# Kernel tuning notes

Hardware: AMD Instinct MI355X
Metric: run time of the kernel (lower is better)

Reference implementation:

```python
import jax, jax.numpy as jnp
import numpy as np

N = 100000
E = 1_600_000
IN_X, OUT_X = 128, 128
IN_E, OUT_E = 32, 128


def setup_inputs() -> dict:
    key = jax.random.key(0)
    k1, k2, k3, k4, k5, k6, k7 = jax.random.split(key, 7)
    x = jax.random.normal(k1, (N, IN_X), dtype=jnp.float32)
    edge_index = jax.random.randint(k2, (2, E), 0, N, dtype=jnp.int64)
    edge_attr = jax.random.normal(k3, (E, IN_E), dtype=jnp.float32)
    Wx = jax.random.normal(k4, (IN_X, OUT_X), dtype=jnp.float32) * (1.0 / np.sqrt(IN_X))
    bx = jax.random.normal(k5, (OUT_X,), dtype=jnp.float32) * 0.01
    We = jax.random.normal(k6, (IN_E, OUT_E), dtype=jnp.float32) * (1.0 / np.sqrt(IN_E))
    be = jax.random.normal(k7, (OUT_E,), dtype=jnp.float32) * 0.01
    return {"x": x, "edge_index": edge_index, "edge_attr": edge_attr,
            "Wx": Wx, "bx": bx, "We": We, "be": be}


def reference(x, edge_index, edge_attr, Wx, bx, We, be):
    # torch: to_dense() -> [N, N, in_e]; sum over dim=1 == scatter-add of
    # edge_attr into rows indexed by the source node edge_index[0].
    agg = jax.ops.segment_sum(edge_attr, edge_index[0], num_segments=x.shape[0])  # [N, in_e]
    hx = x @ Wx + bx          # [N, out_x]
    he = agg @ We + be        # [N, out_e]
    return jnp.concatenate((hx, he), axis=1)  # [N, out_x + out_e]
```

## Files before the change

kernel.cpp:

```cpp
#include <hip/hip_runtime.h>


#define BSHIFT    7
#define BSIZE     128
#define NBMAX     1024
#define SEG_CAP   3584
#define POOL_SZ   3648
#define CHUNK_A   8192
#define SPILL_CAP 65536

typedef short bf16x8 __attribute__((ext_vector_type(8)));
typedef float f32x4  __attribute__((ext_vector_type(4)));

__device__ __forceinline__ unsigned short f2bf(float f) {
    union { float f; unsigned u; } c; c.f = f;
    unsigned u = c.u;
    u += 0x7FFF + ((u >> 16) & 1);
    return (unsigned short)(u >> 16);
}

__global__ __launch_bounds__(512) void binA_kernel(
    const int* __restrict__ src, int E, int nb,
    unsigned* __restrict__ segs, int* __restrict__ gcnt,
    int2* __restrict__ spill, int* __restrict__ spillcnt)
{
    __shared__ unsigned pool[CHUNK_A];
    __shared__ int hist[NBMAX];
    __shared__ int offs[NBMAX];
    __shared__ int lcur[NBMAX];
    __shared__ int gbase[NBMAX];
    __shared__ int gallow[NBMAX];
    __shared__ int wsum[8];

    int tid = threadIdx.x;
    int base = blockIdx.x * CHUNK_A;

    for (int i = tid; i < NBMAX; i += 512) hist[i] = 0;
    __syncthreads();

    int srcv[CHUNK_A / 512];
    #pragma unroll
    for (int u = 0; u < CHUNK_A / 512; ++u) {
        int e = base + tid + u * 512;
        int s = (e < E) ? src[e] : -1;
        srcv[u] = s;
        if (s >= 0) atomicAdd(&hist[s >> BSHIFT], 1);
    }
    __syncthreads();

    {
        int t2 = tid * 2;
        int c0 = hist[t2], c1 = hist[t2 + 1];
        int s = c0 + c1;
        int lane = tid & 63, wid = tid >> 6;
        int ws = s;
        #pragma unroll
        for (int d = 1; d < 64; d <<= 1) {
            int t = __shfl_up(ws, d);
            if (lane >= d) ws += t;
        }
        if (lane == 63) wsum[wid] = ws;
        __syncthreads();
        int woff = 0;
        #pragma unroll
        for (int w = 0; w < 8; ++w) if (w < wid) woff += wsum[w];
        int ex = woff + ws - s;
        offs[t2] = ex;          lcur[t2] = ex;
        offs[t2 + 1] = ex + c0; lcur[t2 + 1] = ex + c0;
    }
    __syncthreads();

    {
        int t2 = tid * 2;
        #pragma unroll
        for (int u = 0; u < 2; ++u) {
            int b = t2 + u;
            if (b < nb) {
                int cnt = hist[b];
                int b0 = cnt ? atomicAdd(&gcnt[b], cnt) : 0;
                gbase[b] = b0;
                int allow = SEG_CAP - b0;
                if (allow < 0) allow = 0;
                if (allow > cnt) allow = cnt;
                gallow[b] = allow;
            }
        }
    }
    __syncthreads();

    #pragma unroll
    for (int u = 0; u < CHUNK_A / 512; ++u) {
        int s = srcv[u];
        if (s >= 0) {
            int e = base + tid + u * 512;
            int b = s >> BSHIFT;
            int p = atomicAdd(&lcur[b], 1);
            pool[p] = ((unsigned)e << BSHIFT) | (unsigned)(s & (BSIZE - 1));
        }
    }
    __syncthreads();

    int wid = tid >> 6, lane = tid & 63;
    for (int b = wid; b < nb; b += 8) {
        int cnt = hist[b];
        int off = offs[b];
        int allow = gallow[b];
        unsigned* dst = segs + (size_t)b * SEG_CAP + gbase[b];
        for (int i = lane; i < allow; i += 64)
            dst[i] = pool[off + i];
        int excess = cnt - allow;
        if (excess > 0) {
            int sb;
            if (lane == 0) sb = atomicAdd(spillcnt, excess);
            sb = __shfl(sb, 0);
            for (int i = lane; i < excess; i += 64) {
                int sp = sb + i;
                if (sp < SPILL_CAP) {
                    unsigned pv = pool[off + allow + i];
                    spill[sp] = make_int2((int)(pv >> BSHIFT),
                                          (b << BSHIFT) | (int)(pv & (BSIZE - 1)));
                }
            }
        }
    }
}

__global__ __launch_bounds__(512, 4) void fused_kernel(
    const unsigned* __restrict__ segs, const int* __restrict__ gcnt,
    const int2* __restrict__ spill, const int* __restrict__ spillcnt,
    const float4* __restrict__ ea4, const float* __restrict__ x,
    const float* __restrict__ Wx, const float* __restrict__ bx,
    const float* __restrict__ We, const float* __restrict__ be,
    float* __restrict__ out, int N)
{
    __shared__ int counts[BSIZE];
    __shared__ int starts[BSIZE + 1];
    __shared__ int cursor[BSIZE];
    __shared__ int pool[POOL_SZ];
    __shared__ char sAgg[BSIZE * 64];
    __shared__ char sWeT[128 * 64];
    __shared__ char sWxT[128 * 256];

    int tid = threadIdx.x;
    int b = blockIdx.x;
    int node0 = b << BSHIFT;
    int lane = tid & 63, w = tid >> 6;
    int col = lane & 15, m = lane >> 4;

    if (tid < BSIZE) counts[tid] = 0;
    for (int i = tid; i < 128 * 128; i += 512) {
        int k = i >> 7, j = i & 127;
        *(unsigned short*)(sWxT + j * 256 + ((k * 2) ^ ((j & 7) << 4))) = f2bf(Wx[i]);
    }
    for (int i = tid; i < 32 * 128; i += 512) {
        int k = i >> 7, j = i & 127;
        *(unsigned short*)(sWeT + j * 64 + ((k * 2) ^ ((j & 3) << 4))) = f2bf(We[i]);
    }
    float bxv[8], bev[8];
    #pragma unroll
    for (int ct = 0; ct < 8; ++ct) {
        bxv[ct] = bx[ct * 16 + col];
        bev[ct] = be[ct * 16 + col];
    }
    __syncthreads();

    int segn = gcnt[b]; if (segn > SEG_CAP) segn = SEG_CAP;
    const unsigned* seg = segs + (size_t)b * SEG_CAP;
    int nsp = *spillcnt; if (nsp > SPILL_CAP) nsp = SPILL_CAP;

    for (int i = tid; i < segn; i += 512)
        atomicAdd(&counts[seg[i] & (BSIZE - 1)], 1);
    if (nsp)
        for (int i = tid; i < nsp; i += 512) {
            int2 p = spill[i];
            if ((p.y >> BSHIFT) == b) atomicAdd(&counts[p.y & (BSIZE - 1)], 1);
        }
    __syncthreads();

    if (tid < 64) {
        int c0 = counts[tid * 2], c1 = counts[tid * 2 + 1];
        int s = c0 + c1;
        int ws = s;
        #pragma unroll
        for (int d = 1; d < 64; d <<= 1) {
            int t = __shfl_up(ws, d);
            if (tid >= d) ws += t;
        }
        int ex = ws - s;
        starts[tid * 2] = ex;          cursor[tid * 2] = ex;
        starts[tid * 2 + 1] = ex + c0; cursor[tid * 2 + 1] = ex + c0;
        if (tid == 63) starts[BSIZE] = ws;
    }
    __syncthreads();

    for (int i = tid; i < segn; i += 512) {
        unsigned pe = seg[i];
        int pos = atomicAdd(&cursor[pe & (BSIZE - 1)], 1);
        if (pos < POOL_SZ) pool[pos] = (int)(pe >> BSHIFT);
    }
    if (nsp)
        for (int i = tid; i < nsp; i += 512) {
            int2 p = spill[i];
            if ((p.y >> BSHIFT) == b) {
                int pos = atomicAdd(&cursor[p.y & (BSIZE - 1)], 1);
                if (pos < POOL_SZ) pool[pos] = p.x;
            }
        }
    __syncthreads();

    {
        int g = tid >> 2, q2 = tid & 3;
        int node = node0 + g;
        float4 aL0 = {0.f,0.f,0.f,0.f}, aL1 = {0.f,0.f,0.f,0.f};
        float4 aH0 = {0.f,0.f,0.f,0.f}, aH1 = {0.f,0.f,0.f,0.f};
        if (node < N) {
            int p0 = starts[g], p1 = starts[g + 1];
            if (p1 > POOL_SZ) p1 = POOL_SZ;
            int p = p0;
            for (; p + 4 <= p1; p += 4) {
                int e0 = pool[p], e1 = pool[p + 1], e2 = pool[p + 2], e3 = pool[p + 3];
                const float4* r0 = ea4 + (size_t)e0 * 8;
                const float4* r1 = ea4 + (size_t)e1 * 8;
                const float4* r2 = ea4 + (size_t)e2 * 8;
                const float4* r3 = ea4 + (size_t)e3 * 8;
                float4 l0 = r0[q2],     l1 = r1[q2],     l2 = r2[q2],     l3 = r3[q2];
                float4 h0 = r0[q2 + 4], h1 = r1[q2 + 4], h2 = r2[q2 + 4], h3 = r3[q2 + 4];
                aL0.x += l0.x; aL0.y += l0.y; aL0.z += l0.z; aL0.w += l0.w;
                aL1.x += l1.x; aL1.y += l1.y; aL1.z += l1.z; aL1.w += l1.w;
                aH0.x += h0.x; aH0.y += h0.y; aH0.z += h0.z; aH0.w += h0.w;
                aH1.x += h1.x; aH1.y += h1.y; aH1.z += h1.z; aH1.w += h1.w;
                aL0.x += l2.x; aL0.y += l2.y; aL0.z += l2.z; aL0.w += l2.w;
                aL1.x += l3.x; aL1.y += l3.y; aL1.z += l3.z; aL1.w += l3.w;
                aH0.x += h2.x; aH0.y += h2.y; aH0.z += h2.z; aH0.w += h2.w;
                aH1.x += h3.x; aH1.y += h3.y; aH1.z += h3.z; aH1.w += h3.w;
            }
            for (; p < p1; ++p) {
                const float4* r = ea4 + (size_t)pool[p] * 8;
                float4 l = r[q2], h = r[q2 + 4];
                aL0.x += l.x; aL0.y += l.y; aL0.z += l.z; aL0.w += l.w;
                aH0.x += h.x; aH0.y += h.y; aH0.z += h.z; aH0.w += h.w;
            }
            aL0.x += aL1.x; aL0.y += aL1.y; aL0.z += aL1.z; aL0.w += aL1.w;
            aH0.x += aH1.x; aH0.y += aH1.y; aH0.z += aH1.z; aH0.w += aH1.w;
        }
        uint2 lo, hi;
        lo.x = (unsigned)f2bf(aL0.x) | ((unsigned)f2bf(aL0.y) << 16);
        lo.y = (unsigned)f2bf(aL0.z) | ((unsigned)f2bf(aL0.w) << 16);
        hi.x = (unsigned)f2bf(aH0.x) | ((unsigned)f2bf(aH0.y) << 16);
        hi.y = (unsigned)f2bf(aH0.z) | ((unsigned)f2bf(aH0.w) << 16);
        int swz = (g & 7) << 4;
        *(uint2*)(sAgg + ((g * 64 + q2 * 8) ^ swz))       = lo;
        *(uint2*)(sAgg + ((g * 64 + (q2 + 4) * 8) ^ swz)) = hi;
    }

    int lrow = (w << 4) + col;
    int grow = node0 + lrow;
    bool rok = grow < N;
    int srow = node0 + (w << 4) + m * 4;

    {
        const float* xr = x + (size_t)grow * 128 + m * 8;
        bf16x8 ax[4];
        #pragma unroll
        for (int kk = 0; kk < 4; ++kk) {
            float4 p0 = {0.f,0.f,0.f,0.f}, p1 = {0.f,0.f,0.f,0.f};
            if (rok) {
                p0 = *(const float4*)(xr + kk * 32);
                p1 = *(const float4*)(xr + kk * 32 + 4);
            }
            bf16x8 a;
            a[0] = (short)f2bf(p0.x); a[1] = (short)f2bf(p0.y);
            a[2] = (short)f2bf(p0.z); a[3] = (short)f2bf(p0.w);
            a[4] = (short)f2bf(p1.x); a[5] = (short)f2bf(p1.y);
            a[6] = (short)f2bf(p1.z); a[7] = (short)f2bf(p1.w);
            ax[kk] = a;
        }

        #pragma unroll
        for (int half = 0; half < 2; ++half) {
            f32x4 acc[4];
            #pragma unroll
            for (int ct = 0; ct < 4; ++ct) {
                int c8 = half * 4 + ct;
                acc[ct] = (f32x4){bxv[c8], bxv[c8], bxv[c8], bxv[c8]};
            }
            #pragma unroll
            for (int ct = 0; ct < 4; ++ct) {
                int c8 = half * 4 + ct;
                const char* brow = sWxT + (c8 * 16 + col) * 256;
                int swz = (col & 7) << 4;
                #pragma unroll
                for (int kk = 0; kk < 4; ++kk) {
                    bf16x8 bfrag = *(const bf16x8*)(brow + ((kk * 64 + m * 16) ^ swz));
                    acc[ct] = __builtin_amdgcn_mfma_f32_16x16x32_bf16(ax[kk], bfrag, acc[ct], 0, 0, 0);
                }
            }
            #pragma unroll
            for (int r = 0; r < 4; ++r) {
                if (srow + r < N) {
                    float* orow = out + (size_t)(srow + r) * 256 + col + half * 64;
                    #pragma unroll
                    for (int ct = 0; ct < 4; ++ct)
                        orow[ct * 16] = acc[ct][r];
                }
            }
        }
    }

    __syncthreads();

    {
        bf16x8 aa = *(const bf16x8*)(sAgg + ((lrow * 64 + m * 16) ^ ((lrow & 7) << 4)));

        f32x4 acc[8];
        #pragma unroll
        for (int ct = 0; ct < 8; ++ct)
            acc[ct] = (f32x4){bev[ct], bev[ct], bev[ct], bev[ct]};
        #pragma unroll
        for (int ct = 0; ct < 8; ++ct) {
            bf16x8 bwe = *(const bf16x8*)(sWeT + (ct * 16 + col) * 64 + ((m * 16) ^ ((col & 3) << 4)));
            acc[ct] = __builtin_amdgcn_mfma_f32_16x16x32_bf16(aa, bwe, acc[ct], 0, 0, 0);
        }

        #pragma unroll
        for (int r = 0; r < 4; ++r) {
            if (srow + r < N) {
                float* orow = out + (size_t)(srow + r) * 256 + 128 + col;
                #pragma unroll
                for (int ct = 0; ct < 8; ++ct)
                    orow[ct * 16] = acc[ct][r];
            }
        }
    }
}

__global__ __launch_bounds__(256) void scatter_kernel(
    const float4* __restrict__ ea4, const int* __restrict__ src,
    float* __restrict__ agg, int nquads)
{
    int t = blockIdx.x * blockDim.x + threadIdx.x;
    if (t >= nquads) return;
    int e = t >> 3, q = t & 7;
    float4 v = ea4[t];
    int node = src[e];
    float* dst = agg + (size_t)node * 32 + q * 4;
    atomicAdd(dst + 0, v.x); atomicAdd(dst + 1, v.y);
    atomicAdd(dst + 2, v.z); atomicAdd(dst + 3, v.w);
}

__global__ __launch_bounds__(256) void cvt_kernel(
    const float* __restrict__ agg, unsigned short* __restrict__ aggbf, int n)
{
    int t = blockIdx.x * blockDim.x + threadIdx.x;
    if (t < n) aggbf[t] = f2bf(agg[t]);
}

__global__ __launch_bounds__(512, 4) void mfma_gemm_full(
    const float* __restrict__ x, const unsigned short* __restrict__ aggbf,
    const float* __restrict__ Wx, const float* __restrict__ bx,
    const float* __restrict__ We, const float* __restrict__ be,
    float* __restrict__ out, int N, int ntiles)
{
    __shared__ char sWxT[128 * 256];
    __shared__ char sWeT[128 * 64];
    __shared__ char sX[128 * 256];
    __shared__ char sA[128 * 64];

    int tid = threadIdx.x;
    int lane = tid & 63, w = tid >> 6;
    int col = lane & 15, m = lane >> 4;

    for (int i = tid; i < 128 * 128; i += 512) {
        int k = i >> 7, j = i & 127;
        *(unsigned short*)(sWxT + j * 256 + ((k * 2) ^ ((j & 7) << 4))) = f2bf(Wx[i]);
    }
    for (int i = tid; i < 32 * 128; i += 512) {
        int k = i >> 7, j = i & 127;
        *(unsigned short*)(sWeT + j * 64 + ((k * 2) ^ ((j & 3) << 4))) = f2bf(We[i]);
    }
    float bxv[8], bev[8];
    #pragma unroll
    for (int ct = 0; ct < 8; ++ct) {
        bxv[ct] = bx[ct * 16 + col];
        bev[ct] = be[ct * 16 + col];
    }

    int lrow = (w << 4) + col;
    int swzA = (lrow & 7) << 4;

    for (int t = blockIdx.x; t < ntiles; t += gridDim.x) {
        int rbase_t = t << 7;
        __syncthreads();

        for (int i = tid; i < 128 * 32; i += 512) {
            int row = i >> 5, c4 = i & 31;
            int gr = rbase_t + row;
            float4 v = {0.f, 0.f, 0.f, 0.f};
            if (gr < N) v = *(const float4*)(x + (size_t)gr * 128 + c4 * 4);
            uint2 uu;
            uu.x = (unsigned)f2bf(v.x) | ((unsigned)f2bf(v.y) << 16);
            uu.y = (unsigned)f2bf(v.z) | ((unsigned)f2bf(v.w) << 16);
            *(uint2*)(sX + ((row * 256 + c4 * 8) ^ ((row & 7) << 4))) = uu;
        }
        {
            int row = tid >> 2, mm = tid & 3;
            int gr = rbase_t + row;
            bf16x8 av = {0, 0, 0, 0, 0, 0, 0, 0};
            if (gr < N) av = *(const bf16x8*)(aggbf + (size_t)gr * 32 + mm * 8);
            *(bf16x8*)(sA + ((row * 64 + mm * 16) ^ ((row & 7) << 4))) = av;
        }
        __syncthreads();

        bf16x8 ax[4];
        #pragma unroll
        for (int kk = 0; kk < 4; ++kk)
            ax[kk] = *(const bf16x8*)(sX + lrow * 256 + ((kk * 64 + m * 16) ^ swzA));
        bf16x8 aa = *(const bf16x8*)(sA + ((lrow * 64 + m * 16) ^ swzA));

        int srow = rbase_t + (w << 4) + m * 4;

        #pragma unroll
        for (int half = 0; half < 2; ++half) {
            f32x4 acc[8];
            #pragma unroll
            for (int ct = 0; ct < 4; ++ct) {
                int c8 = half * 4 + ct;
                acc[ct]     = (f32x4){bxv[c8], bxv[c8], bxv[c8], bxv[c8]};
                acc[4 + ct] = (f32x4){bev[c8], bev[c8], bev[c8], bev[c8]};
            }
            #pragma unroll
            for (int ct = 0; ct < 4; ++ct) {
                int c8 = half * 4 + ct;
                const char* brow = sWxT + (c8 * 16 + col) * 256;
                int swz = (col & 7) << 4;
                #pragma unroll
                for (int kk = 0; kk < 4; ++kk) {
                    bf16x8 bfrag = *(const bf16x8*)(brow + ((kk * 64 + m * 16) ^ swz));
                    acc[ct] = __builtin_amdgcn_mfma_f32_16x16x32_bf16(ax[kk], bfrag, acc[ct], 0, 0, 0);
                }
                bf16x8 bwe = *(const bf16x8*)(sWeT + (c8 * 16 + col) * 64 + ((m * 16) ^ ((col & 3) << 4)));
                acc[4 + ct] = __builtin_amdgcn_mfma_f32_16x16x32_bf16(aa, bwe, acc[4 + ct], 0, 0, 0);
            }
            #pragma unroll
            for (int r = 0; r < 4; ++r) {
                if (srow + r < N) {
                    float* orow = out + (size_t)(srow + r) * 256 + col + half * 64;
                    #pragma unroll
                    for (int ct = 0; ct < 4; ++ct) {
                        orow[ct * 16]       = acc[ct][r];
                        orow[128 + ct * 16] = acc[4 + ct][r];
                    }
                }
            }
        }
    }
}

extern "C" void kernel_launch(void* const* d_in, const int* in_sizes, int n_in,
                              void* d_out, int out_size, void* d_ws, size_t ws_size,
                              hipStream_t stream) {
    const float* x          = (const float*)d_in[0];
    const int*   edge_index = (const int*)d_in[1];
    const float* edge_attr  = (const float*)d_in[2];
    const float* Wx         = (const float*)d_in[3];
    const float* bx         = (const float*)d_in[4];
    const float* We         = (const float*)d_in[5];
    const float* be         = (const float*)d_in[6];
    float* out = (float*)d_out;

    int N = in_sizes[0] / 128;
    int E = in_sizes[2] / 32;
    int nb = (N + BSIZE - 1) >> BSHIFT;
    int ntiles = (N + 127) >> 7;

    char* ws = (char*)d_ws;
    size_t aggbfBytes = ((size_t)N * 32 * 2 + 255) & ~255ull;
    size_t segsBytes  = ((size_t)nb * SEG_CAP * 4 + 255) & ~255ull;
    size_t gcntBytes  = ((size_t)(nb + 1) * 4 + 255) & ~255ull;
    size_t spillBytes = (size_t)SPILL_CAP * 8;
    size_t need = aggbfBytes + segsBytes + gcntBytes + spillBytes;

    unsigned short* aggbf = (unsigned short*)ws;

    if (ws_size >= need && nb <= NBMAX) {
        unsigned* segs  = (unsigned*)(ws + aggbfBytes);
        int* gcnt       = (int*)(ws + aggbfBytes + segsBytes);
        int* spillcnt   = gcnt + nb;
        int2* spill     = (int2*)(ws + aggbfBytes + segsBytes + gcntBytes);

        hipMemsetAsync(gcnt, 0, (size_t)(nb + 1) * 4, stream);
        int nblkA = (E + CHUNK_A - 1) / CHUNK_A;
        binA_kernel<<<nblkA, 512, 0, stream>>>(edge_index, E, nb, segs, gcnt, spill, spillcnt);
        fused_kernel<<<nb, 512, 0, stream>>>(segs, gcnt, spill, spillcnt,
                                             (const float4*)edge_attr, x,
                                             Wx, bx, We, be, out, N);
    } else {
        float* aggf = (float*)(ws + aggbfBytes);
        hipMemsetAsync(aggf, 0, (size_t)N * 32 * 4, stream);
        int nq = E * 8;
        scatter_kernel<<<(nq + 255) / 256, 256, 0, stream>>>(
            (const float4*)edge_attr, edge_index, aggf, nq);
        cvt_kernel<<<(N * 32 + 255) / 256, 256, 0, stream>>>(aggf, aggbf, N * 32);
        int g = ntiles < 512 ? ntiles : 512;
        mfma_gemm_full<<<g, 512, 0, stream>>>(x, aggbf, Wx, bx, We, be, out, N, ntiles);
    }
}
```

Measured before the change: 147.2 us.

## Warp-specialize fused kernel: half gathers edges, half runs x GEMM; stage segs in LDS

```diff
diff --git a/kernel.cpp b/kernel.cpp
--- a/kernel.cpp
+++ b/kernel.cpp
@@ -17,6 +17,10 @@
     unsigned u = c.u;
     u += 0x7FFF + ((u >> 16) & 1);
     return (unsigned short)(u >> 16);
+}
+
+__device__ __forceinline__ void acc4(float4& a, const float4 v) {
+    a.x += v.x; a.y += v.y; a.z += v.z; a.w += v.w;
 }
 
 __global__ __launch_bounds__(512) void binA_kernel(
@@ -136,6 +140,7 @@
     __shared__ int counts[BSIZE];
     __shared__ int starts[BSIZE + 1];
     __shared__ int cursor[BSIZE];
+    __shared__ unsigned spool[SEG_CAP];
     __shared__ int pool[POOL_SZ];
     __shared__ char sAgg[BSIZE * 64];
     __shared__ char sWeT[128 * 64];
@@ -147,6 +152,10 @@
     int lane = tid & 63, w = tid >> 6;
     int col = lane & 15, m = lane >> 4;
 
+    int segn = gcnt[b]; if (segn > SEG_CAP) segn = SEG_CAP;
+    const unsigned* seg = segs + (size_t)b * SEG_CAP;
+    int nsp = *spillcnt; if (nsp > SPILL_CAP) nsp = SPILL_CAP;
+
     if (tid < BSIZE) counts[tid] = 0;
     for (int i = tid; i < 128 * 128; i += 512) {
         int k = i >> 7, j = i & 127;
@@ -156,6 +165,7 @@
         int k = i >> 7, j = i & 127;
         *(unsigned short*)(sWeT + j * 64 + ((k * 2) ^ ((j & 3) << 4))) = f2bf(We[i]);
     }
+    for (int i = tid; i < segn; i += 512) spool[i] = seg[i];
     float bxv[8], bev[8];
     #pragma unroll
     for (int ct = 0; ct < 8; ++ct) {
@@ -164,12 +174,8 @@
     }
     __syncthreads();
 
-    int segn = gcnt[b]; if (segn > SEG_CAP) segn = SEG_CAP;
-    const unsigned* seg = segs + (size_t)b * SEG_CAP;
-    int nsp = *spillcnt; if (nsp > SPILL_CAP) nsp = SPILL_CAP;
-
     for (int i = tid; i < segn; i += 512)
-        atomicAdd(&counts[seg[i] & (BSIZE - 1)], 1);
+        atomicAdd(&counts[spool[i] & (BSIZE - 1)], 1);
     if (nsp)
         for (int i = tid; i < nsp; i += 512) {
             int2 p = spill[i];
@@ -194,7 +200,7 @@
     __syncthreads();
 
     for (int i = tid; i < segn; i += 512) {
-        unsigned pe = seg[i];
+        unsigned pe = spool[i];
         int pos = atomicAdd(&cursor[pe & (BSIZE - 1)], 1);
         if (pos < POOL_SZ) pool[pos] = (int)(pe >> BSHIFT);
     }
@@ -208,100 +214,106 @@
         }
     __syncthreads();
 
-    {
-        int g = tid >> 2, q2 = tid & 3;
+    int srow = node0 + (w << 4) + m * 4;
+    int lrow = (w << 4) + col;
+
+    if (tid < 256) {
+        int g = tid >> 1;
+        int h = (tid & 1) * 4;
         int node = node0 + g;
-        float4 aL0 = {0.f,0.f,0.f,0.f}, aL1 = {0.f,0.f,0.f,0.f};
-        float4 aH0 = {0.f,0.f,0.f,0.f}, aH1 = {0.f,0.f,0.f,0.f};
+        float4 a0 = {0.f,0.f,0.f,0.f}, a1 = {0.f,0.f,0.f,0.f};
+        float4 a2 = {0.f,0.f,0.f,0.f}, a3 = {0.f,0.f,0.f,0.f};
+        float4 c0 = {0.f,0.f,0.f,0.f}, c1 = {0.f,0.f,0.f,0.f};
+        float4 c2 = {0.f,0.f,0.f,0.f}, c3 = {0.f,0.f,0.f,0.f};
         if (node < N) {
             int p0 = starts[g], p1 = starts[g + 1];
             if (p1 > POOL_SZ) p1 = POOL_SZ;
             int p = p0;
             for (; p + 4 <= p1; p += 4) {
-                int e0 = pool[p], e1 = pool[p + 1], e2 = pool[p + 2], e3 = pool[p + 3];
-                const float4* r0 = ea4 + (size_t)e0 * 8;
-                const float4* r1 = ea4 + (size_t)e1 * 8;
-                const float4* r2 = ea4 + (size_t)e2 * 8;
-                const float4* r3 = ea4 + (size_t)e3 * 8;
-                float4 l0 = r0[q2],     l1 = r1[q2],     l2 = r2[q2],     l3 = r3[q2];
-                float4 h0 = r0[q2 + 4], h1 = r1[q2 + 4], h2 = r2[q2 + 4], h3 = r3[q2 + 4];
-                aL0.x += l0.x; aL0.y += l0.y; aL0.z += l0.z; aL0.w += l0.w;
-                aL1.x += l1.x; aL1.y += l1.y; aL1.z += l1.z; aL1.w += l1.w;
-                aH0.x += h0.x; aH0.y += h0.y; aH0.z += h0.z; aH0.w += h0.w;
-                aH1.x += h1.x; aH1.y += h1.y; aH1.z += h1.z; aH1.w += h1.w;
-                aL0.x += l2.x; aL0.y += l2.y; aL0.z += l2.z; aL0.w += l2.w;
-                aL1.x += l3.x; aL1.y += l3.y; aL1.z += l3.z; aL1.w += l3.w;
-                aH0.x += h2.x; aH0.y += h2.y; aH0.z += h2.z; aH0.w += h2.w;
-                aH1.x += h3.x; aH1.y += h3.y; aH1.z += h3.z; aH1.w += h3.w;
+                const float4* r0 = ea4 + (size_t)pool[p]     * 8 + h;
+                const float4* r1 = ea4 + (size_t)pool[p + 1] * 8 + h;
+                const float4* r2 = ea4 + (size_t)pool[p + 2] * 8 + h;
+                const float4* r3 = ea4 + (size_t)pool[p + 3] * 8 + h;
+                float4 v00 = r0[0], v01 = r0[1], v02 = r0[2], v03 = r0[3];
+                float4 v10 = r1[0], v11 = r1[1], v12 = r1[2], v13 = r1[3];
+                float4 v20 = r2[0], v21 = r2[1], v22 = r2[2], v23 = r2[3];
+                float4 v30 = r3[0], v31 = r3[1], v32 = r3[2], v33 = r3[3];
+                acc4(a0, v00); acc4(a1, v01); acc4(a2, v02); acc4(a3, v03);
+                acc4(c0, v10); acc4(c1, v11); acc4(c2, v12); acc4(c3, v13);
+                acc4(a0, v20); acc4(a1, v21); acc4(a2, v22); acc4(a3, v23);
+                acc4(c0, v30); acc4(c1, v31); acc4(c2, v32); acc4(c3, v33);
             }
             for (; p < p1; ++p) {
-                const float4* r = ea4 + (size_t)pool[p] * 8;
-                float4 l = r[q2], h = r[q2 + 4];
-                aL0.x += l.x; aL0.y += l.y; aL0.z += l.z; aL0.w += l.w;
-                aH0.x += h.x; aH0.y += h.y; aH0.z += h.z; aH0.w += h.w;
-            }
-            aL0.x += aL1.x; aL0.y += aL1.y; aL0.z += aL1.z; aL0.w += aL1.w;
-            aH0.x += aH1.x; aH0.y += aH1.y; aH0.z += aH1.z; aH0.w += aH1.w;
-        }
-        uint2 lo, hi;
-        lo.x = (unsigned)f2bf(aL0.x) | ((unsigned)f2bf(aL0.y) << 16);
-        lo.y = (unsigned)f2bf(aL0.z) | ((unsigned)f2bf(aL0.w) << 16);
-        hi.x = (unsigned)f2bf(aH0.x) | ((unsigned)f2bf(aH0.y) << 16);
-        hi.y = (unsigned)f2bf(aH0.z) | ((unsigned)f2bf(aH0.w) << 16);
+                const float4* r = ea4 + (size_t)pool[p] * 8 + h;
+                acc4(a0, r[0]); acc4(a1, r[1]); acc4(a2, r[2]); acc4(a3, r[3]);
+            }
+            acc4(a0, c0); acc4(a1, c1); acc4(a2, c2); acc4(a3, c3);
+        }
         int swz = (g & 7) << 4;
-        *(uint2*)(sAgg + ((g * 64 + q2 * 8) ^ swz))       = lo;
-        *(uint2*)(sAgg + ((g * 64 + (q2 + 4) * 8) ^ swz)) = hi;
-    }
-
-    int lrow = (w << 4) + col;
-    int grow = node0 + lrow;
-    bool rok = grow < N;
-    int srow = node0 + (w << 4) + m * 4;
-
-    {
-        const float* xr = x + (size_t)grow * 128 + m * 8;
-        bf16x8 ax[4];
-        #pragma unroll
-        for (int kk = 0; kk < 4; ++kk) {
-            float4 p0 = {0.f,0.f,0.f,0.f}, p1 = {0.f,0.f,0.f,0.f};
-            if (rok) {
-                p0 = *(const float4*)(xr + kk * 32);
-                p1 = *(const float4*)(xr + kk * 32 + 4);
-            }
-            bf16x8 a;
-            a[0] = (short)f2bf(p0.x); a[1] = (short)f2bf(p0.y);
-            a[2] = (short)f2bf(p0.z); a[3] = (short)f2bf(p0.w);
-            a[4] = (short)f2bf(p1.x); a[5] = (short)f2bf(p1.y);
-            a[6] = (short)f2bf(p1.z); a[7] = (short)f2bf(p1.w);
-            ax[kk] = a;
-        }
-
-        #pragma unroll
-        for (int half = 0; half < 2; ++half) {
-            f32x4 acc[4];
+        uint2 u0, u1, u2, u3;
+        u0.x = (unsigned)f2bf(a0.x) | ((unsigned)f2bf(a0.y) << 16);
+        u0.y = (unsigned)f2bf(a0.z) | ((unsigned)f2bf(a0.w) << 16);
+        u1.x = (unsigned)f2bf(a1.x) | ((unsigned)f2bf(a1.y) << 16);
+        u1.y = (unsigned)f2bf(a1.z) | ((unsigned)f2bf(a1.w) << 16);
+        u2.x = (unsigned)f2bf(a2.x) | ((unsigned)f2bf(a2.y) << 16);
+        u2.y = (unsigned)f2bf(a2.z) | ((unsigned)f2bf(a2.w) << 16);
+        u3.x = (unsigned)f2bf(a3.x) | ((unsigned)f2bf(a3.y) << 16);
+        u3.y = (unsigned)f2bf(a3.z) | ((unsigned)f2bf(a3.w) << 16);
+        *(uint2*)(sAgg + ((g * 64 + (h + 0) * 8) ^ swz)) = u0;
+        *(uint2*)(sAgg + ((g * 64 + (h + 1) * 8) ^ swz)) = u1;
+        *(uint2*)(sAgg + ((g * 64 + (h + 2) * 8) ^ swz)) = u2;
+        *(uint2*)(sAgg + ((g * 64 + (h + 3) * 8) ^ swz)) = u3;
+    } else {
+        int tt2 = (w - 4) * 2;
+        #pragma unroll
+        for (int s = 0; s < 2; ++s) {
+            int tt = tt2 + s;
+            int grow = node0 + tt * 16 + col;
+            bool rok = grow < N;
+            const float* xr = x + (size_t)grow * 128 + m * 8;
+            bf16x8 ax[4];
             #pragma unroll
-            for (int ct = 0; ct < 4; ++ct) {
-                int c8 = half * 4 + ct;
-                acc[ct] = (f32x4){bxv[c8], bxv[c8], bxv[c8], bxv[c8]};
-            }
+            for (int kk = 0; kk < 4; ++kk) {
+                float4 p0 = {0.f,0.f,0.f,0.f}, p1 = {0.f,0.f,0.f,0.f};
+                if (rok) {
+                    p0 = *(const float4*)(xr + kk * 32);
+                    p1 = *(const float4*)(xr + kk * 32 + 4);
+                }
+                bf16x8 a;
+                a[0] = (short)f2bf(p0.x); a[1] = (short)f2bf(p0.y);
+                a[2] = (short)f2bf(p0.z); a[3] = (short)f2bf(p0.w);
+                a[4] = (short)f2bf(p1.x); a[5] = (short)f2bf(p1.y);
+                a[6] = (short)f2bf(p1.z); a[7] = (short)f2bf(p1.w);
+                ax[kk] = a;
+            }
+            int str = node0 + tt * 16 + m * 4;
             #pragma unroll
-            for (int ct = 0; ct < 4; ++ct) {
-                int c8 = half * 4 + ct;
-                const char* brow = sWxT + (c8 * 16 + col) * 256;
-                int swz = (col & 7) << 4;
+            for (int half = 0; half < 2; ++half) {
+                f32x4 acc[4];
                 #pragma unroll
-                for (int kk = 0; kk < 4; ++kk) {
-                    bf16x8 bfrag = *(const bf16x8*)(brow + ((kk * 64 + m * 16) ^ swz));
-                    acc[ct] = __builtin_amdgcn_mfma_f32_16x16x32_bf16(ax[kk], bfrag, acc[ct], 0, 0, 0);
-                }
-            }
-            #pragma unroll
-            for (int r = 0; r < 4; ++r) {
-                if (srow + r < N) {
-                    float* orow = out + (size_t)(srow + r) * 256 + col + half * 64;
+                for (int ct = 0; ct < 4; ++ct) {
+                    int c8 = half * 4 + ct;
+                    acc[ct] = (f32x4){bxv[c8], bxv[c8], bxv[c8], bxv[c8]};
+                }
+                #pragma unroll
+                for (int ct = 0; ct < 4; ++ct) {
+                    int c8 = half * 4 + ct;
+                    const char* brow = sWxT + (c8 * 16 + col) * 256;
+                    int swz = (col & 7) << 4;
                     #pragma unroll
-                    for (int ct = 0; ct < 4; ++ct)
-                        orow[ct * 16] = acc[ct][r];
+                    for (int kk = 0; kk < 4; ++kk) {
+                        bf16x8 bfrag = *(const bf16x8*)(brow + ((kk * 64 + m * 16) ^ swz));
+                        acc[ct] = __builtin_amdgcn_mfma_f32_16x16x32_bf16(ax[kk], bfrag, acc[ct], 0, 0, 0);
+                    }
+                }
+                #pragma unroll
+                for (int r = 0; r < 4; ++r) {
+                    if (str + r < N) {
+                        float* orow = out + (size_t)(str + r) * 256 + col + half * 64;
+                        #pragma unroll
+                        for (int ct = 0; ct < 4; ++ct)
+                            orow[ct * 16] = acc[ct][r];
+                    }
                 }
             }
         }
```

New measurement: 181.9 us. 1.24x slower.

## Precompute bf16 transposed weights once and read them from global memory instead of LDS

Applied to the files above, without the earlier changes.

```diff
diff --git a/kernel.cpp b/kernel.cpp
--- a/kernel.cpp
+++ b/kernel.cpp
@@ -17,6 +17,25 @@
     unsigned u = c.u;
     u += 0x7FFF + ((u >> 16) & 1);
     return (unsigned short)(u >> 16);
+}
+
+__device__ __forceinline__ void acc4(float4& a, const float4 v) {
+    a.x += v.x; a.y += v.y; a.z += v.z; a.w += v.w;
+}
+
+__global__ __launch_bounds__(256) void prep_kernel(
+    const float* __restrict__ Wx, const float* __restrict__ We,
+    unsigned short* __restrict__ WxT, unsigned short* __restrict__ WeT)
+{
+    int t = blockIdx.x * 256 + threadIdx.x;
+    if (t < 128 * 128) {
+        int j = t >> 7, k = t & 127;
+        WxT[j * 128 + k] = f2bf(Wx[k * 128 + j]);
+    }
+    if (t < 128 * 32) {
+        int j = t >> 5, k = t & 31;
+        WeT[j * 32 + k] = f2bf(We[k * 128 + j]);
+    }
 }
 
 __global__ __launch_bounds__(512) void binA_kernel(
@@ -125,12 +144,12 @@
     }
 }
 
-__global__ __launch_bounds__(512, 4) void fused_kernel(
+__global__ __launch_bounds__(512, 8) void fused_kernel(
     const unsigned* __restrict__ segs, const int* __restrict__ gcnt,
     const int2* __restrict__ spill, const int* __restrict__ spillcnt,
     const float4* __restrict__ ea4, const float* __restrict__ x,
-    const float* __restrict__ Wx, const float* __restrict__ bx,
-    const float* __restrict__ We, const float* __restrict__ be,
+    const unsigned short* __restrict__ wxt, const float* __restrict__ bx,
+    const unsigned short* __restrict__ wet, const float* __restrict__ be,
     float* __restrict__ out, int N)
 {
     __shared__ int counts[BSIZE];
@@ -138,8 +157,6 @@
     __shared__ int cursor[BSIZE];
     __shared__ int pool[POOL_SZ];
     __shared__ char sAgg[BSIZE * 64];
-    __shared__ char sWeT[128 * 64];
-    __shared__ char sWxT[128 * 256];
 
     int tid = threadIdx.x;
     int b = blockIdx.x;
@@ -148,20 +165,6 @@
     int col = lane & 15, m = lane >> 4;
 
     if (tid < BSIZE) counts[tid] = 0;
-    for (int i = tid; i < 128 * 128; i += 512) {
-        int k = i >> 7, j = i & 127;
-        *(unsigned short*)(sWxT + j * 256 + ((k * 2) ^ ((j & 7) << 4))) = f2bf(Wx[i]);
-    }
-    for (int i = tid; i < 32 * 128; i += 512) {
-        int k = i >> 7, j = i & 127;
-        *(unsigned short*)(sWeT + j * 64 + ((k * 2) ^ ((j & 3) << 4))) = f2bf(We[i]);
-    }
-    float bxv[8], bev[8];
-    #pragma unroll
-    for (int ct = 0; ct < 8; ++ct) {
-        bxv[ct] = bx[ct * 16 + col];
-        bev[ct] = be[ct * 16 + col];
-    }
     __syncthreads();
 
     int segn = gcnt[b]; if (segn > SEG_CAP) segn = SEG_CAP;
@@ -225,23 +228,15 @@
                 const float4* r3 = ea4 + (size_t)e3 * 8;
                 float4 l0 = r0[q2],     l1 = r1[q2],     l2 = r2[q2],     l3 = r3[q2];
                 float4 h0 = r0[q2 + 4], h1 = r1[q2 + 4], h2 = r2[q2 + 4], h3 = r3[q2 + 4];
-                aL0.x += l0.x; aL0.y += l0.y; aL0.z += l0.z; aL0.w += l0.w;
-                aL1.x += l1.x; aL1.y += l1.y; aL1.z += l1.z; aL1.w += l1.w;
-                aH0.x += h0.x; aH0.y += h0.y; aH0.z += h0.z; aH0.w += h0.w;
-                aH1.x += h1.x; aH1.y += h1.y; aH1.z += h1.z; aH1.w += h1.w;
-                aL0.x += l2.x; aL0.y += l2.y; aL0.z += l2.z; aL0.w += l2.w;
-                aL1.x += l3.x; aL1.y += l3.y; aL1.z += l3.z; aL1.w += l3.w;
-                aH0.x += h2.x; aH0.y += h2.y; aH0.z += h2.z; aH0.w += h2.w;
-                aH1.x += h3.x; aH1.y += h3.y; aH1.z += h3.z; aH1.w += h3.w;
+                acc4(aL0, l0); acc4(aL1, l1); acc4(aH0, h0); acc4(aH1, h1);
+                acc4(aL0, l2); acc4(aL1, l3); acc4(aH0, h2); acc4(aH1, h3);
             }
             for (; p < p1; ++p) {
                 const float4* r = ea4 + (size_t)pool[p] * 8;
                 float4 l = r[q2], h = r[q2 + 4];
-                aL0.x += l.x; aL0.y += l.y; aL0.z += l.z; aL0.w += l.w;
-                aH0.x += h.x; aH0.y += h.y; aH0.z += h.z; aH0.w += h.w;
-            }
-            aL0.x += aL1.x; aL0.y += aL1.y; aL0.z += aL1.z; aL0.w += aL1.w;
-            aH0.x += aH1.x; aH0.y += aH1.y; aH0.z += aH1.z; aH0.w += aH1.w;
+                acc4(aL0, l); acc4(aH0, h);
+            }
+            acc4(aL0, aL1); acc4(aH0, aH1);
         }
         uint2 lo, hi;
         lo.x = (unsigned)f2bf(aL0.x) | ((unsigned)f2bf(aL0.y) << 16);
@@ -282,16 +277,16 @@
             #pragma unroll
             for (int ct = 0; ct < 4; ++ct) {
                 int c8 = half * 4 + ct;
-                acc[ct] = (f32x4){bxv[c8], bxv[c8], bxv[c8], bxv[c8]};
+                float bv = bx[c8 * 16 + col];
+                acc[ct] = (f32x4){bv, bv, bv, bv};
             }
             #pragma unroll
             for (int ct = 0; ct < 4; ++ct) {
                 int c8 = half * 4 + ct;
-                const char* brow = sWxT + (c8 * 16 + col) * 256;
-                int swz = (col & 7) << 4;
+                const unsigned short* brow = wxt + (size_t)(c8 * 16 + col) * 128;
                 #pragma unroll
                 for (int kk = 0; kk < 4; ++kk) {
-                    bf16x8 bfrag = *(const bf16x8*)(brow + ((kk * 64 + m * 16) ^ swz));
+                    bf16x8 bfrag = *(const bf16x8*)(brow + kk * 32 + m * 8);
                     acc[ct] = __builtin_amdgcn_mfma_f32_16x16x32_bf16(ax[kk], bfrag, acc[ct], 0, 0, 0);
                 }
             }
@@ -314,11 +309,13 @@
 
         f32x4 acc[8];
         #pragma unroll
-        for (int ct = 0; ct < 8; ++ct)
-            acc[ct] = (f32x4){bev[ct], bev[ct], bev[ct], bev[ct]};
-        #pragma unroll
         for (int ct = 0; ct < 8; ++ct) {
-            bf16x8 bwe = *(const bf16x8*)(sWeT + (ct * 16 + col) * 64 + ((m * 16) ^ ((col & 3) << 4)));
+            float bv = be[ct * 16 + col];
+            acc[ct] = (f32x4){bv, bv, bv, bv};
+        }
+        #pragma unroll
+        for (int ct = 0; ct < 8; ++ct) {
+            bf16x8 bwe = *(const bf16x8*)(wet + (size_t)(ct * 16 + col) * 32 + m * 8);
             acc[ct] = __builtin_amdgcn_mfma_f32_16x16x32_bf16(aa, bwe, acc[ct], 0, 0, 0);
         }
 
@@ -474,28 +471,34 @@
     int ntiles = (N + 127) >> 7;
 
     char* ws = (char*)d_ws;
+    size_t wxtBytes   = 128 * 128 * 2;
+    size_t wetBytes   = 128 * 32 * 2;
     size_t aggbfBytes = ((size_t)N * 32 * 2 + 255) & ~255ull;
     size_t segsBytes  = ((size_t)nb * SEG_CAP * 4 + 255) & ~255ull;
     size_t gcntBytes  = ((size_t)(nb + 1) * 4 + 255) & ~255ull;
     size_t spillBytes = (size_t)SPILL_CAP * 8;
-    size_t need = aggbfBytes + segsBytes + gcntBytes + spillBytes;
-
-    unsigned short* aggbf = (unsigned short*)ws;
+    size_t need = wxtBytes + wetBytes + aggbfBytes + segsBytes + gcntBytes + spillBytes;
+
+    unsigned short* wxt   = (unsigned short*)ws;
+    unsigned short* wet   = (unsigned short*)(ws + wxtBytes);
+    unsigned short* aggbf = (unsigned short*)(ws + wxtBytes + wetBytes);
 
     if (ws_size >= need && nb <= NBMAX) {
-        unsigned* segs  = (unsigned*)(ws + aggbfBytes);
-        int* gcnt       = (int*)(ws + aggbfBytes + segsBytes);
+        char* p = ws + wxtBytes + wetBytes + aggbfBytes;
+        unsigned* segs  = (unsigned*)p;
+        int* gcnt       = (int*)(p + segsBytes);
         int* spillcnt   = gcnt + nb;
-        int2* spill     = (int2*)(ws + aggbfBytes + segsBytes + gcntBytes);
+        int2* spill     = (int2*)(p + segsBytes + gcntBytes);
 
         hipMemsetAsync(gcnt, 0, (size_t)(nb + 1) * 4, stream);
+        prep_kernel<<<64, 256, 0, stream>>>(Wx, We, wxt, wet);
         int nblkA = (E + CHUNK_A - 1) / CHUNK_A;
         binA_kernel<<<nblkA, 512, 0, stream>>>(edge_index, E, nb, segs, gcnt, spill, spillcnt);
         fused_kernel<<<nb, 512, 0, stream>>>(segs, gcnt, spill, spillcnt,
                                              (const float4*)edge_attr, x,
-                                             Wx, bx, We, be, out, N);
+                                             wxt, bx, wet, be, out, N);
     } else {
-        float* aggf = (float*)(ws + aggbfBytes);
+        float* aggf = (float*)(ws + wxtBytes + wetBytes + aggbfBytes);
         hipMemsetAsync(aggf, 0, (size_t)N * 32 * 4, stream);
         int nq = E * 8;
         scatter_kernel<<<(nq + 255) / 256, 256, 0, stream>>>(
```

Result: slower. 183.2 us (+24.4%).

## Split fused kernel into separate aggregate and x-GEMM blocks per tile

Applied to the files above, without the earlier changes.

```diff
diff --git a/kernel.cpp b/kernel.cpp
--- a/kernel.cpp
+++ b/kernel.cpp
@@ -17,6 +17,10 @@
     unsigned u = c.u;
     u += 0x7FFF + ((u >> 16) & 1);
     return (unsigned short)(u >> 16);
+}
+
+__device__ __forceinline__ void acc4(float4& a, const float4 v) {
+    a.x += v.x; a.y += v.y; a.z += v.z; a.w += v.w;
 }
 
 __global__ __launch_bounds__(512) void binA_kernel(
@@ -125,7 +129,7 @@
     }
 }
 
-__global__ __launch_bounds__(512, 4) void fused_kernel(
+__global__ __launch_bounds__(512, 4) void mega_kernel(
     const unsigned* __restrict__ segs, const int* __restrict__ gcnt,
     const int2* __restrict__ spill, const int* __restrict__ spillcnt,
     const float4* __restrict__ ea4, const float* __restrict__ x,
@@ -133,132 +137,151 @@
     const float* __restrict__ We, const float* __restrict__ be,
     float* __restrict__ out, int N)
 {
-    __shared__ int counts[BSIZE];
-    __shared__ int starts[BSIZE + 1];
-    __shared__ int cursor[BSIZE];
-    __shared__ int pool[POOL_SZ];
-    __shared__ char sAgg[BSIZE * 64];
-    __shared__ char sWeT[128 * 64];
-    __shared__ char sWxT[128 * 256];
+    __shared__ __align__(16) char smem[32768];
 
     int tid = threadIdx.x;
-    int b = blockIdx.x;
-    int node0 = b << BSHIFT;
+    int bid = blockIdx.x;
+    int idx = bid >> 1;
     int lane = tid & 63, w = tid >> 6;
     int col = lane & 15, m = lane >> 4;
-
-    if (tid < BSIZE) counts[tid] = 0;
-    for (int i = tid; i < 128 * 128; i += 512) {
-        int k = i >> 7, j = i & 127;
-        *(unsigned short*)(sWxT + j * 256 + ((k * 2) ^ ((j & 7) << 4))) = f2bf(Wx[i]);
-    }
-    for (int i = tid; i < 32 * 128; i += 512) {
-        int k = i >> 7, j = i & 127;
-        *(unsigned short*)(sWeT + j * 64 + ((k * 2) ^ ((j & 3) << 4))) = f2bf(We[i]);
-    }
-    float bxv[8], bev[8];
-    #pragma unroll
-    for (int ct = 0; ct < 8; ++ct) {
-        bxv[ct] = bx[ct * 16 + col];
-        bev[ct] = be[ct * 16 + col];
-    }
-    __syncthreads();
-
-    int segn = gcnt[b]; if (segn > SEG_CAP) segn = SEG_CAP;
-    const unsigned* seg = segs + (size_t)b * SEG_CAP;
-    int nsp = *spillcnt; if (nsp > SPILL_CAP) nsp = SPILL_CAP;
-
-    for (int i = tid; i < segn; i += 512)
-        atomicAdd(&counts[seg[i] & (BSIZE - 1)], 1);
-    if (nsp)
-        for (int i = tid; i < nsp; i += 512) {
-            int2 p = spill[i];
-            if ((p.y >> BSHIFT) == b) atomicAdd(&counts[p.y & (BSIZE - 1)], 1);
-        }
-    __syncthreads();
-
-    if (tid < 64) {
-        int c0 = counts[tid * 2], c1 = counts[tid * 2 + 1];
-        int s = c0 + c1;
-        int ws = s;
-        #pragma unroll
-        for (int d = 1; d < 64; d <<= 1) {
-            int t = __shfl_up(ws, d);
-            if (tid >= d) ws += t;
-        }
-        int ex = ws - s;
-        starts[tid * 2] = ex;          cursor[tid * 2] = ex;
-        starts[tid * 2 + 1] = ex + c0; cursor[tid * 2 + 1] = ex + c0;
-        if (tid == 63) starts[BSIZE] = ws;
-    }
-    __syncthreads();
-
-    for (int i = tid; i < segn; i += 512) {
-        unsigned pe = seg[i];
-        int pos = atomicAdd(&cursor[pe & (BSIZE - 1)], 1);
-        if (pos < POOL_SZ) pool[pos] = (int)(pe >> BSHIFT);
-    }
-    if (nsp)
-        for (int i = tid; i < nsp; i += 512) {
-            int2 p = spill[i];
-            if ((p.y >> BSHIFT) == b) {
-                int pos = atomicAdd(&cursor[p.y & (BSIZE - 1)], 1);
-                if (pos < POOL_SZ) pool[pos] = p.x;
-            }
-        }
-    __syncthreads();
-
-    {
-        int g = tid >> 2, q2 = tid & 3;
-        int node = node0 + g;
-        float4 aL0 = {0.f,0.f,0.f,0.f}, aL1 = {0.f,0.f,0.f,0.f};
-        float4 aH0 = {0.f,0.f,0.f,0.f}, aH1 = {0.f,0.f,0.f,0.f};
-        if (node < N) {
-            int p0 = starts[g], p1 = starts[g + 1];
-            if (p1 > POOL_SZ) p1 = POOL_SZ;
-            int p = p0;
-            for (; p + 4 <= p1; p += 4) {
-                int e0 = pool[p], e1 = pool[p + 1], e2 = pool[p + 2], e3 = pool[p + 3];
-                const float4* r0 = ea4 + (size_t)e0 * 8;
-                const float4* r1 = ea4 + (size_t)e1 * 8;
-                const float4* r2 = ea4 + (size_t)e2 * 8;
-                const float4* r3 = ea4 + (size_t)e3 * 8;
-                float4 l0 = r0[q2],     l1 = r1[q2],     l2 = r2[q2],     l3 = r3[q2];
-                float4 h0 = r0[q2 + 4], h1 = r1[q2 + 4], h2 = r2[q2 + 4], h3 = r3[q2 + 4];
-                aL0.x += l0.x; aL0.y += l0.y; aL0.z += l0.z; aL0.w += l0.w;
-                aL1.x += l1.x; aL1.y += l1.y; aL1.z += l1.z; aL1.w += l1.w;
-                aH0.x += h0.x; aH0.y += h0.y; aH0.z += h0.z; aH0.w += h0.w;
-                aH1.x += h1.x; aH1.y += h1.y; aH1.z += h1.z; aH1.w += h1.w;
-                aL0.x += l2.x; aL0.y += l2.y; aL0.z += l2.z; aL0.w += l2.w;
-                aL1.x += l3.x; aL1.y += l3.y; aL1.z += l3.z; aL1.w += l3.w;
-                aH0.x += h2.x; aH0.y += h2.y; aH0.z += h2.z; aH0.w += h2.w;
-                aH1.x += h3.x; aH1.y += h3.y; aH1.z += h3.z; aH1.w += h3.w;
-            }
-            for (; p < p1; ++p) {
-                const float4* r = ea4 + (size_t)pool[p] * 8;
-                float4 l = r[q2], h = r[q2 + 4];
-                aL0.x += l.x; aL0.y += l.y; aL0.z += l.z; aL0.w += l.w;
-                aH0.x += h.x; aH0.y += h.y; aH0.z += h.z; aH0.w += h.w;
-            }
-            aL0.x += aL1.x; aL0.y += aL1.y; aL0.z += aL1.z; aL0.w += aL1.w;
-            aH0.x += aH1.x; aH0.y += aH1.y; aH0.z += aH1.z; aH0.w += aH1.w;
-        }
-        uint2 lo, hi;
-        lo.x = (unsigned)f2bf(aL0.x) | ((unsigned)f2bf(aL0.y) << 16);
-        lo.y = (unsigned)f2bf(aL0.z) | ((unsigned)f2bf(aL0.w) << 16);
-        hi.x = (unsigned)f2bf(aH0.x) | ((unsigned)f2bf(aH0.y) << 16);
-        hi.y = (unsigned)f2bf(aH0.z) | ((unsigned)f2bf(aH0.w) << 16);
-        int swz = (g & 7) << 4;
-        *(uint2*)(sAgg + ((g * 64 + q2 * 8) ^ swz))       = lo;
-        *(uint2*)(sAgg + ((g * 64 + (q2 + 4) * 8) ^ swz)) = hi;
-    }
-
+    int node0 = idx << BSHIFT;
+    int srow = node0 + (w << 4) + m * 4;
     int lrow = (w << 4) + col;
-    int grow = node0 + lrow;
-    bool rok = grow < N;
-    int srow = node0 + (w << 4) + m * 4;
-
-    {
+
+    if ((bid & 1) == 0) {
+        int* pool   = (int*)smem;
+        int* counts = (int*)(smem + 14592);
+        int* starts = (int*)(smem + 15104);
+        int* cursor = (int*)(smem + 15624);
+        char* sAgg  = smem + 16384;
+        char* sWeT  = smem + 24576;
+
+        int b = idx;
+        if (tid < BSIZE) counts[tid] = 0;
+        for (int i = tid; i < 32 * 128; i += 512) {
+            int k = i >> 7, j = i & 127;
+            *(unsigned short*)(sWeT + j * 64 + ((k * 2) ^ ((j & 3) << 4))) = f2bf(We[i]);
+        }
+        __syncthreads();
+
+        int segn = gcnt[b]; if (segn > SEG_CAP) segn = SEG_CAP;
+        const unsigned* seg = segs + (size_t)b * SEG_CAP;
+        int nsp = *spillcnt; if (nsp > SPILL_CAP) nsp = SPILL_CAP;
+
+        for (int i = tid; i < segn; i += 512)
+            atomicAdd(&counts[seg[i] & (BSIZE - 1)], 1);
+        if (nsp)
+            for (int i = tid; i < nsp; i += 512) {
+                int2 p = spill[i];
+                if ((p.y >> BSHIFT) == b) atomicAdd(&counts[p.y & (BSIZE - 1)], 1);
+            }
+        __syncthreads();
+
+        if (tid < 64) {
+            int c0 = counts[tid * 2], c1 = counts[tid * 2 + 1];
+            int s = c0 + c1;
+            int ws = s;
+            #pragma unroll
+            for (int d = 1; d < 64; d <<= 1) {
+                int t = __shfl_up(ws, d);
+                if (tid >= d) ws += t;
+            }
+            int ex = ws - s;
+            starts[tid * 2] = ex;          cursor[tid * 2] = ex;
+            starts[tid * 2 + 1] = ex + c0; cursor[tid * 2 + 1] = ex + c0;
+            if (tid == 63) starts[BSIZE] = ws;
+        }
+        __syncthreads();
+
+        for (int i = tid; i < segn; i += 512) {
+            unsigned pe = seg[i];
+            int pos = atomicAdd(&cursor[pe & (BSIZE - 1)], 1);
+            if (pos < POOL_SZ) pool[pos] = (int)(pe >> BSHIFT);
+        }
+        if (nsp)
+            for (int i = tid; i < nsp; i += 512) {
+                int2 p = spill[i];
+                if ((p.y >> BSHIFT) == b) {
+                    int pos = atomicAdd(&cursor[p.y & (BSIZE - 1)], 1);
+                    if (pos < POOL_SZ) pool[pos] = p.x;
+                }
+            }
+        __syncthreads();
+
+        {
+            int g = tid >> 2, q2 = tid & 3;
+            int node = node0 + g;
+            float4 aL0 = {0.f,0.f,0.f,0.f}, aL1 = {0.f,0.f,0.f,0.f};
+            float4 aH0 = {0.f,0.f,0.f,0.f}, aH1 = {0.f,0.f,0.f,0.f};
+            if (node < N) {
+                int p0 = starts[g], p1 = starts[g + 1];
+                if (p1 > POOL_SZ) p1 = POOL_SZ;
+                int p = p0;
+                for (; p + 4 <= p1; p += 4) {
+                    int e0 = pool[p], e1 = pool[p + 1], e2 = pool[p + 2], e3 = pool[p + 3];
+                    const float4* r0 = ea4 + (size_t)e0 * 8;
+                    const float4* r1 = ea4 + (size_t)e1 * 8;
+                    const float4* r2 = ea4 + (size_t)e2 * 8;
+                    const float4* r3 = ea4 + (size_t)e3 * 8;
+                    float4 l0 = r0[q2],     l1 = r1[q2],     l2 = r2[q2],     l3 = r3[q2];
+                    float4 h0 = r0[q2 + 4], h1 = r1[q2 + 4], h2 = r2[q2 + 4], h3 = r3[q2 + 4];
+                    acc4(aL0, l0); acc4(aL1, l1); acc4(aH0, h0); acc4(aH1, h1);
+                    acc4(aL0, l2); acc4(aL1, l3); acc4(aH0, h2); acc4(aH1, h3);
+                }
+                for (; p < p1; ++p) {
+                    const float4* r = ea4 + (size_t)pool[p] * 8;
+                    float4 l = r[q2], h = r[q2 + 4];
+                    acc4(aL0, l); acc4(aH0, h);
+                }
+                acc4(aL0, aL1); acc4(aH0, aH1);
+            }
+            uint2 lo, hi;
+            lo.x = (unsigned)f2bf(aL0.x) | ((unsigned)f2bf(aL0.y) << 16);
+            lo.y = (unsigned)f2bf(aL0.z) | ((unsigned)f2bf(aL0.w) << 16);
+            hi.x = (unsigned)f2bf(aH0.x) | ((unsigned)f2bf(aH0.y) << 16);
+            hi.y = (unsigned)f2bf(aH0.z) | ((unsigned)f2bf(aH0.w) << 16);
+            int swz = (g & 7) << 4;
+            *(uint2*)(sAgg + ((g * 64 + q2 * 8) ^ swz))       = lo;
+            *(uint2*)(sAgg + ((g * 64 + (q2 + 4) * 8) ^ swz)) = hi;
+        }
+        __syncthreads();
+
+        {
+            bf16x8 aa = *(const bf16x8*)(sAgg + ((lrow * 64 + m * 16) ^ ((lrow & 7) << 4)));
+
+            f32x4 acc[8];
+            #pragma unroll
+            for (int ct = 0; ct < 8; ++ct) {
+                float bv = be[ct * 16 + col];
+                acc[ct] = (f32x4){bv, bv, bv, bv};
+            }
+            #pragma unroll
+            for (int ct = 0; ct < 8; ++ct) {
+                bf16x8 bwe = *(const bf16x8*)(sWeT + (ct * 16 + col) * 64 + ((m * 16) ^ ((col & 3) << 4)));
+                acc[ct] = __builtin_amdgcn_mfma_f32_16x16x32_bf16(aa, bwe, acc[ct], 0, 0, 0);
+            }
+            #pragma unroll
+            for (int r = 0; r < 4; ++r) {
+                if (srow + r < N) {
+                    float* orow = out + (size_t)(srow + r) * 256 + 128 + col;
+                    #pragma unroll
+                    for (int ct = 0; ct < 8; ++ct)
+                        orow[ct * 16] = acc[ct][r];
+                }
+            }
+        }
+    } else {
+        char* sWxT = smem;
+
+        for (int i = tid; i < 128 * 128; i += 512) {
+            int k = i >> 7, j = i & 127;
+            *(unsigned short*)(sWxT + j * 256 + ((k * 2) ^ ((j & 7) << 4))) = f2bf(Wx[i]);
+        }
+        __syncthreads();
+
+        int grow = node0 + lrow;
+        bool rok = grow < N;
+
         const float* xr = x + (size_t)grow * 128 + m * 8;
         bf16x8 ax[4];
         #pragma unroll
@@ -282,7 +305,8 @@
             #pragma unroll
             for (int ct = 0; ct < 4; ++ct) {
                 int c8 = half * 4 + ct;
-                acc[ct] = (f32x4){bxv[c8], bxv[c8], bxv[c8], bxv[c8]};
+                float bv = bx[c8 * 16 + col];
+                acc[ct] = (f32x4){bv, bv, bv, bv};
             }
             #pragma unroll
             for (int ct = 0; ct < 4; ++ct) {
@@ -303,32 +327,6 @@
                     for (int ct = 0; ct < 4; ++ct)
                         orow[ct * 16] = acc[ct][r];
                 }
-            }
-        }
-    }
-
-    __syncthreads();
-
-    {
-        bf16x8 aa = *(const bf16x8*)(sAgg + ((lrow * 64 + m * 16) ^ ((lrow & 7) << 4)));
-
-        f32x4 acc[8];
-        #pragma unroll
-        for (int ct = 0; ct < 8; ++ct)
-            acc[ct] = (f32x4){bev[ct], bev[ct], bev[ct], bev[ct]};
-        #pragma unroll
-        for (int ct = 0; ct < 8; ++ct) {
-            bf16x8 bwe = *(const bf16x8*)(sWeT + (ct * 16 + col) * 64 + ((m * 16) ^ ((col & 3) << 4)));
-            acc[ct] = __builtin_amdgcn_mfma_f32_16x16x32_bf16(aa, bwe, acc[ct], 0, 0, 0);
-        }
-
-        #pragma unroll
-        for (int r = 0; r < 4; ++r) {
-            if (srow + r < N) {
-                float* orow = out + (size_t)(srow + r) * 256 + 128 + col;
-                #pragma unroll
-                for (int ct = 0; ct < 8; ++ct)
-                    orow[ct * 16] = acc[ct][r];
             }
         }
     }
@@ -491,9 +489,9 @@
         hipMemsetAsync(gcnt, 0, (size_t)(nb + 1) * 4, stream);
         int nblkA = (E + CHUNK_A - 1) / CHUNK_A;
         binA_kernel<<<nblkA, 512, 0, stream>>>(edge_index, E, nb, segs, gcnt, spill, spillcnt);
-        fused_kernel<<<nb, 512, 0, stream>>>(segs, gcnt, spill, spillcnt,
-                                             (const float4*)edge_attr, x,
-                                             Wx, bx, We, be, out, N);
+        mega_kernel<<<2 * nb, 512, 0, stream>>>(segs, gcnt, spill, spillcnt,
+                                                (const float4*)edge_attr, x,
+                                                Wx, bx, We, be, out, N);
     } else {
         float* aggf = (float*)(ws + aggbfBytes);
         hipMemsetAsync(aggf, 0, (size_t)N * 32 * 4, stream);
```

New measurement: 141.6 us. -3.8%, faster.
